# Performance work log

Hardware: AMD Instinct MI355X
Metric: run time of the kernel (lower is better)

## Reference

```python
import jax, jax.numpy as jnp
import numpy as np

NHEAD, DK, DV = 8, 32, 32
GRAPH = [[1,2,3,6,7],[1,2,4],[1,3,5],[2,4],[3,5],[1,6,8,12],[1,7,9,13],[6,8,10],[7,9,13],[8,10],[9,11],[9,12,14],[11,13,15],[12,14,16],[13,15,17],[14,16],[15,17]]
_idx = np.zeros((17,5), np.int32); _val = np.zeros((17,5), bool)
for _i, _nb in enumerate(GRAPH):
    for _j, _n in enumerate(_nb):
        _idx[_i,_j] = _n-1; _val[_i,_j] = True
NBR_IDX = jnp.asarray(_idx)            # (17,5) neighbor table (pad idx 0)
NBR_VALID = jnp.asarray(_val)          # (17,5) valid-neighbor mask
ATT_MASK = jnp.asarray(np.concatenate([_val, np.ones((17,2), bool)], 1))  # (17,7): 5 local + 2 global keys
INV_SQRT_DK = float(1.0/np.sqrt(DK))

def _ln_c(x, g, b, eps=1e-6):
    # LayerNorm over channel axis of (B,C,L)
    m = x.mean(1, keepdims=True)
    v = x.var(1, keepdims=True)
    return (x - m) * jax.lax.rsqrt(v + eps) * g[None,:,None] + b[None,:,None]

def _bn3(x, g, b, eps=1e-5):
    # BatchNorm1d (training batch stats) per channel over (B,L); x:(B,C,L)
    m = x.mean((0,2), keepdims=True)
    v = x.var((0,2), keepdims=True)
    return (x - m) * jax.lax.rsqrt(v + eps) * g[None,:,None] + b[None,:,None]

def _pos_ffn(x, w1, b1, w2, b2, g, b):
    # x:(B,C,L); Linear over C, relu, Linear back, residual, BatchNorm1d
    h = jax.nn.relu(jnp.einsum('bcl,hc->bhl', x, w1) + b1[None,:,None])
    y = jnp.einsum('bhl,ch->bcl', h, w2) + b2[None,:,None] + x
    return _bn3(y, g, b)

def _unfold(t):
    # t:(B,C,17) -> (B,C,5,17): per-node 5-wide neighbor window, zero padded
    g = t[:,:,NBR_IDX]                              # (B,C,17,5)
    g = jnp.where(NBR_VALID[None,None], g, 0.0)
    return jnp.transpose(g, (0,1,3,2))

def _sju(xn, ax, wq,bq,wk,bk,wv,bv, bng,bnb, f1w,f1b,f2w,f2b,fg,fb):
    B, C, L = xn.shape
    q = (jnp.einsum('oc,bcl->bol', wq, xn) + bq[None,:,None]).reshape(B,NHEAD,DK,L)
    kx = jnp.einsum('oc,bcl->bol', wk, xn) + bk[None,:,None]
    vx = jnp.einsum('oc,bcl->bol', wv, xn) + bv[None,:,None]
    k = _unfold(kx).reshape(B,NHEAD,DK,5,L)
    v = _unfold(vx).reshape(B,NHEAD,DV,5,L)
    ak = (jnp.einsum('oc,bcal->boal', wk, ax) + bk[None,:,None,None]).reshape(B,NHEAD,DK,2,L)
    av = (jnp.einsum('oc,bcal->boal', wv, ax) + bv[None,:,None,None]).reshape(B,NHEAD,DV,2,L)
    k = jnp.concatenate([k, ak], 3)                 # (B,H,dk,7,L)
    v = jnp.concatenate([v, av], 3)
    pre = jnp.einsum('bhdl,bhdwl->bhwl', q, k) * INV_SQRT_DK
    pre = jnp.where(ATT_MASK.T[None,None], pre, -jnp.inf)
    a = jax.nn.softmax(pre, axis=2)
    att = jnp.einsum('bhwl,bhdwl->bhdl', a, v).reshape(B,C,L)
    ret = _bn3(xn + att, bng, bnb)
    return _pos_ffn(ret, f1w,f1b,f2w,f2b,fg,fb)

def _sru(x, y, wq,bq,wk,bk,wv,bv, bng,bnb, f1w,f1b,f2w,f2b,fg,fb):
    # x:(B,C) relay, y:(B,C,Ly) keys/values
    B, C = x.shape
    q = (x @ wq.T + bq).reshape(B,NHEAD,DK)
    k = (jnp.einsum('oc,bcl->bol', wk, y) + bk[None,:,None]).reshape(B,NHEAD,DK,-1)
    v = (jnp.einsum('oc,bcl->bol', wv, y) + bv[None,:,None]).reshape(B,NHEAD,DV,-1)
    a = jax.nn.softmax(jnp.einsum('bhd,bhdl->bhl', q, k) * INV_SQRT_DK, axis=2)
    att = jnp.einsum('bhl,bhdl->bhd', a, v).reshape(B,C)
    ret = _bn3((x + att)[:,:,None], bng, bnb)
    return _pos_ffn(ret, f1w,f1b,f2w,f2b,fg,fb)[:,:,0]

def _forward(data, ln_g, ln_b, jq_w, jq_b, jk_w, jk_b, jv_w, jv_b, jbn_g, jbn_b, jf1_w, jf1_b, jf2_w, jf2_b, jfbn_g, jfbn_b, rq_w, rq_b, rk_w, rk_b, rv_w, rv_b, rbn_g, rbn_b, rf1_w, rf1_b, rf2_w, rf2_b, rfbn_g, rfbn_b):
    B, C, V, T = data.shape
    embs = jnp.transpose(data, (0,3,1,2)).reshape(B*T, C, V)   # fold time into batch
    nodes = embs
    relay = embs.mean(2)                                       # (BT,C)
    # ax: per node the 2 extra keys = its own original embedding + relay (fixed across layers)
    ax = jnp.stack([embs, jnp.broadcast_to(relay[:,:,None], embs.shape)], axis=2)  # (BT,C,2,V)
    for i in range(ln_g.shape[0]):
        xn = _ln_c(nodes, ln_g[i], ln_b[i])
        nodes = jax.nn.leaky_relu(_sju(xn, ax, jq_w[i],jq_b[i],jk_w[i],jk_b[i],jv_w[i],jv_b[i],jbn_g[i],jbn_b[i],jf1_w[i],jf1_b[i],jf2_w[i],jf2_b[i],jfbn_g[i],jfbn_b[i]), 0.01)
        y = jnp.concatenate([relay[:,:,None], nodes], axis=2)   # (BT,C,18)
        relay = jax.nn.leaky_relu(_sru(relay, y, rq_w[i],rq_b[i],rk_w[i],rk_b[i],rv_w[i],rv_b[i],rbn_g[i],rbn_b[i],rf1_w[i],rf1_b[i],rf2_w[i],rf2_b[i],rfbn_g[i],rfbn_b[i]), 0.01)
    return jnp.transpose(nodes.reshape(B,T,C,V), (0,2,3,1))

def setup_inputs():
    key = jax.random.key(0)
    Lyr, C, DIN, B, T, V = 2, 256, 1024, 4, 256, 17
    ks = jax.random.split(key, 40)
    ctr = [0]
    def nxt():
        k = ks[ctr[0]]; ctr[0] += 1; return k
    def w(shape, s=0.05):
        return jax.random.normal(nxt(), shape, jnp.float32) * s
    ones = lambda: jnp.ones((Lyr, C), jnp.float32)
    zeros = lambda: jnp.zeros((Lyr, C), jnp.float32)
    inp = {'data': jax.random.normal(nxt(), (B,C,V,T), jnp.float32),
           'ln_g': ones(), 'ln_b': zeros()}
    for p in ('j', 'r'):
        inp[p+'q_w'] = w((Lyr,C,C)); inp[p+'q_b'] = w((Lyr,C))
        inp[p+'k_w'] = w((Lyr,C,C)); inp[p+'k_b'] = w((Lyr,C))
        inp[p+'v_w'] = w((Lyr,C,C)); inp[p+'v_b'] = w((Lyr,C))
        inp[p+'bn_g'] = ones(); inp[p+'bn_b'] = zeros()
        inp[p+'f1_w'] = w((Lyr,DIN,C)); inp[p+'f1_b'] = w((Lyr,DIN))
        inp[p+'f2_w'] = w((Lyr,C,DIN)); inp[p+'f2_b'] = w((Lyr,C))
        inp[p+'fbn_g'] = ones(); inp[p+'fbn_b'] = zeros()
    return inp

def reference(data, ln_g, ln_b, jq_w, jq_b, jk_w, jk_b, jv_w, jv_b, jbn_g, jbn_b, jf1_w, jf1_b, jf2_w, jf2_b, jfbn_g, jfbn_b, rq_w, rq_b, rk_w, rk_b, rv_w, rv_b, rbn_g, rbn_b, rf1_w, rf1_b, rf2_w, rf2_b, rfbn_g, rfbn_b):
    return _forward(data, ln_g, ln_b, jq_w, jq_b, jk_w, jk_b, jv_w, jv_b, jbn_g, jbn_b, jf1_w, jf1_b, jf2_w, jf2_b, jfbn_g, jfbn_b, rq_w, rq_b, rk_w, rk_b, rv_w, rv_b, rbn_g, rbn_b, rf1_w, rf1_b, rf2_w, rf2_b, rfbn_g, rfbn_b)
```

## Files before the change

### kernel.cpp

```cpp
#include <hip/hip_runtime.h>
#include <hip/hip_bf16.h>


using bf16 = __hip_bfloat16;
typedef __attribute__((ext_vector_type(8))) short bf16x8v;
typedef __attribute__((ext_vector_type(4))) float f32x4;

namespace {
constexpr int kBT = 1024;
constexpr int kC = 256;
constexpr int kV = 17;
constexpr int kT = 256;
constexpr int kDIN = 1024;
constexpr int kRows = kBT * kV;
constexpr int kRowsE = kRows + kBT;
constexpr float kInvSqrtDk = 0.17677669529663687f;
constexpr size_t SZ_BIG = (size_t)kRows * kC;
}

__constant__ int c_nbi[17][5] = {
    {0, 1, 2, 5, 6},   {0, 1, 3, 0, 0},   {0, 2, 4, 0, 0},  {1, 3, 0, 0, 0},
    {2, 4, 0, 0, 0},   {0, 5, 7, 11, 0},  {0, 6, 8, 12, 0}, {5, 7, 9, 0, 0},
    {6, 8, 12, 0, 0},  {7, 9, 0, 0, 0},   {8, 10, 0, 0, 0}, {8, 11, 13, 0, 0},
    {10, 12, 14, 0, 0},{11, 13, 15, 0, 0},{12, 14, 16, 0, 0},
    {13, 15, 0, 0, 0}, {14, 16, 0, 0, 0}};
__constant__ int c_ncnt[17] = {5, 3, 3, 2, 2, 4, 4, 3, 3, 2, 2, 3, 3, 3, 3, 2, 2};

__device__ inline float bf2f(unsigned short s) {
  unsigned int u = ((unsigned int)s) << 16;
  float f;
  __builtin_memcpy(&f, &u, 4);
  return f;
}
__device__ inline unsigned short f2bf(float f) {
  unsigned int u;
  __builtin_memcpy(&u, &f, 4);
  unsigned int r = (u + 0x7fffu + ((u >> 16) & 1u)) >> 16;
  return (unsigned short)r;
}
__device__ inline float4 ldbf4(const bf16* p) {
  ushort4 u = *(const ushort4*)p;
  return make_float4(bf2f(u.x), bf2f(u.y), bf2f(u.z), bf2f(u.w));
}
__device__ inline void stbf4(bf16* p, float4 v) {
  ushort4 u = make_ushort4(f2bf(v.x), f2bf(v.y), f2bf(v.z), f2bf(v.w));
  *(ushort4*)p = u;
}
__device__ inline float dot4(float4 a, float4 b) {
  return a.x * b.x + a.y * b.y + a.z * b.z + a.w * b.w;
}

__device__ inline void async16(const bf16* g, bf16* l) {
  __builtin_amdgcn_global_load_lds(
      (const __attribute__((address_space(1))) void*)g,
      (__attribute__((address_space(3))) void*)l, 16, 0, 0);
}

__global__ __launch_bounds__(256) void k_mfma_gemm(
    const bf16* __restrict__ A, const bf16* __restrict__ W,
    const float* __restrict__ bias, const float* __restrict__ res,
    float* __restrict__ outF, bf16* __restrict__ outB,
    int M, int N, int K, int flags) {
  __shared__ bf16 As[128 * 128];
  __shared__ bf16 Bs[128 * 128];
  const int tid = threadIdx.x;
  const int wave = tid >> 6;
  const int lane = tid & 63;
  const int row0 = blockIdx.x * 128;
  const int col0 = blockIdx.y * 128;

  const int sub = lane >> 2;
  const int kq = (lane & 3) * 8;
  const int rg0 = (2 * wave + 0) * 16;
  const int rg1 = (2 * wave + 1) * 16;
  const bf16* ag0 = A + (size_t)(row0 + rg0 + sub) * K + kq;
  const bf16* ag1 = A + (size_t)(row0 + rg1 + sub) * K + kq;
  const bf16* bg0 = W + (size_t)(col0 + rg0 + sub) * K + kq;
  const bf16* bg1 = W + (size_t)(col0 + rg1 + sub) * K + kq;

  const int wm = wave >> 1, wn = wave & 1;
  const int fr = lane & 15;
  const int fk = (lane >> 4) * 8;

  f32x4 acc[4][4];
#pragma unroll
  for (int i = 0; i < 4; ++i)
#pragma unroll
    for (int j = 0; j < 4; ++j) acc[i][j] = (f32x4){0.f, 0.f, 0.f, 0.f};

  for (int k0 = 0; k0 < K; k0 += 128) {
    if (k0) __syncthreads();
#pragma unroll
    for (int kc = 0; kc < 4; ++kc) {
      const int off = k0 + kc * 32;
      async16(ag0 + off, &As[kc * 4096 + rg0 * 32]);
      async16(ag1 + off, &As[kc * 4096 + rg1 * 32]);
      async16(bg0 + off, &Bs[kc * 4096 + rg0 * 32]);
      async16(bg1 + off, &Bs[kc * 4096 + rg1 * 32]);
    }
    __syncthreads();
#pragma unroll
    for (int kc = 0; kc < 4; ++kc) {
      bf16x8v af[4], bfv[4];
#pragma unroll
      for (int i = 0; i < 4; ++i)
        af[i] =
            *(const bf16x8v*)&As[kc * 4096 + (wm * 64 + i * 16 + fr) * 32 + fk];
#pragma unroll
      for (int j = 0; j < 4; ++j)
        bfv[j] =
            *(const bf16x8v*)&Bs[kc * 4096 + (wn * 64 + j * 16 + fr) * 32 + fk];
#pragma unroll
      for (int i = 0; i < 4; ++i)
#pragma unroll
        for (int j = 0; j < 4; ++j)
          acc[i][j] = __builtin_amdgcn_mfma_f32_16x16x32_bf16(af[i], bfv[j],
                                                              acc[i][j], 0, 0,
                                                              0);
    }
  }

  if (flags & 4) {
    unsigned short* cs = (unsigned short*)As;
    __syncthreads();
#pragma unroll
    for (int j = 0; j < 4; ++j) {
      int lc = wn * 64 + j * 16 + fr;
      float bv = bias ? bias[col0 + lc] : 0.f;
#pragma unroll
      for (int i = 0; i < 4; ++i) {
        int lr = wm * 64 + i * 16 + (lane >> 4) * 4;
#pragma unroll
        for (int r = 0; r < 4; ++r) {
          float v = acc[i][j][r] + bv;
          if (flags & 1) v = fmaxf(v, 0.f);
          cs[(lr + r) * 128 + lc] = f2bf(v);
        }
      }
    }
    __syncthreads();
#pragma unroll
    for (int p = 0; p < 8; ++p) {
      int lr = p * 16 + (tid >> 4);
      int lc = (tid & 15) * 8;
      *(bf16x8v*)&outB[(size_t)(row0 + lr) * N + col0 + lc] =
          *(const bf16x8v*)&cs[lr * 128 + lc];
    }
  } else {
    const int crow = row0 + wm * 64;
    const int ccol = col0 + wn * 64;
#pragma unroll
    for (int j = 0; j < 4; ++j) {
      int col = ccol + j * 16 + fr;
      float bv = bias ? bias[col] : 0.f;
#pragma unroll
      for (int i = 0; i < 4; ++i) {
        int rowb = crow + i * 16 + (lane >> 4) * 4;
#pragma unroll
        for (int r = 0; r < 4; ++r) {
          size_t row = (size_t)(rowb + r);
          float v = acc[i][j][r] + bv;
          if (res) v += res[row * N + col];
          if (flags & 1) v = fmaxf(v, 0.f);
          outF[row * N + col] = v;
        }
      }
    }
  }
}

__global__ __launch_bounds__(256) void k_xform_in(const float* __restrict__ data,
                                                  float* __restrict__ nodes,
                                                  bf16* __restrict__ embs_bf) {
  __shared__ float tile[32][33];
  int ct = blockIdx.x * 32, tt = blockIdx.y * 32;
  int bv = blockIdx.z;
  int b = bv / kV, v = bv - b * kV;
  int tx = threadIdx.x & 31, ty = threadIdx.x >> 5;
  for (int i = ty; i < 32; i += 8)
    tile[i][tx] = data[(((size_t)b * kC + ct + i) * kV + v) * kT + tt + tx];
  __syncthreads();
  for (int i = ty; i < 32; i += 8) {
    size_t s = (size_t)b * kT + tt + i;
    size_t idx = (s * kV + v) * kC + ct + tx;
    float val = tile[tx][i];
    nodes[idx] = val;
    embs_bf[idx] = __float2bfloat16(val);
  }
}

__global__ __launch_bounds__(256) void k_xform_out(const float* __restrict__ nodes,
                                                   float* __restrict__ out) {
  __shared__ float tile[32][33];
  int ct = blockIdx.x * 32, tt = blockIdx.y * 32;
  int bv = blockIdx.z;
  int b = bv / kV, v = bv - b * kV;
  int tx = threadIdx.x & 31, ty = threadIdx.x >> 5;
  for (int i = ty; i < 32; i += 8) {
    size_t s = (size_t)b * kT + tt + i;
    tile[i][tx] = nodes[(s * kV + v) * kC + ct + tx];
  }
  __syncthreads();
  for (int i = ty; i < 32; i += 8)
    out[(((size_t)b * kC + ct + i) * kV + v) * kT + tt + tx] = tile[tx][i];
}

__global__ __launch_bounds__(256) void k_relay_init(const float* __restrict__ nodes,
                                                    bf16* __restrict__ relay0_bf) {
  int t = threadIdx.x;
  int s = blockIdx.x * 4 + (t >> 6);
  int c4 = (t & 63) * 4;
  float4 acc = make_float4(0.f, 0.f, 0.f, 0.f);
#pragma unroll
  for (int v = 0; v < kV; ++v) {
    float4 x = *(const float4*)(nodes + ((size_t)s * kV + v) * kC + c4);
    acc.x += x.x; acc.y += x.y; acc.z += x.z; acc.w += x.w;
  }
  float4 r = make_float4(acc.x / 17.f, acc.y / 17.f, acc.z / 17.f, acc.w / 17.f);
  stbf4(relay0_bf + (size_t)s * kC + c4, r);
}

__global__ __launch_bounds__(256) void k_layernorm(const float* __restrict__ X,
                                                   const float* __restrict__ g,
                                                   const float* __restrict__ b,
                                                   float* __restrict__ O,
                                                   bf16* __restrict__ Ob) {
  int t = threadIdx.x;
  int row = blockIdx.x * 4 + (t >> 6);
  int c4 = (t & 63) * 4;
  size_t i = (size_t)row * kC + c4;
  float4 x = *(const float4*)(X + i);
  float s = x.x + x.y + x.z + x.w;
  float q = dot4(x, x);
#pragma unroll
  for (int o = 32; o >= 1; o >>= 1) {
    s += __shfl_xor(s, o);
    q += __shfl_xor(q, o);
  }
  float m = s * (1.f / 256.f);
  float var = q * (1.f / 256.f) - m * m;
  float rs = rsqrtf(var + 1e-6f);
  float4 g4 = *(const float4*)(g + c4);
  float4 b4 = *(const float4*)(b + c4);
  float4 o4 = make_float4((x.x - m) * rs * g4.x + b4.x,
                          (x.y - m) * rs * g4.y + b4.y,
                          (x.z - m) * rs * g4.z + b4.z,
                          (x.w - m) * rs * g4.w + b4.w);
  *(float4*)(O + i) = o4;
  stbf4(Ob + i, o4);
}

__global__ __launch_bounds__(256) void k_attn_sat(const bf16* __restrict__ qkv,
                                                  const bf16* __restrict__ akav,
                                                  float* __restrict__ z) {
  int t = threadIdx.x;
  int rl = blockIdx.x * 4 + (t >> 6);
  int lane = t & 63;
  int s = rl / kV, l = rl - s * kV;
  int c4 = lane * 4;
  float4 q = ldbf4(qkv + (size_t)rl * 768 + c4);
  int cnt = c_ncnt[l];
  float sc[7];
  int nrow[5];
#pragma unroll
  for (int w = 0; w < 5; ++w) {
    nrow[w] = s * kV + c_nbi[l][w];
    float4 k = ldbf4(qkv + (size_t)nrow[w] * 768 + 256 + c4);
    float p = dot4(q, k);
    p += __shfl_xor(p, 1, 8);
    p += __shfl_xor(p, 2, 8);
    p += __shfl_xor(p, 4, 8);
    sc[w] = (w < cnt) ? p * kInvSqrtDk : -1e30f;
  }
  {
    float4 k = ldbf4(akav + (size_t)rl * 1024 + c4);
    float p = dot4(q, k);
    p += __shfl_xor(p, 1, 8);
    p += __shfl_xor(p, 2, 8);
    p += __shfl_xor(p, 4, 8);
    sc[5] = p * kInvSqrtDk;
  }
  {
    float4 k = ldbf4(akav + (size_t)(kRows + s) * 1024 + c4);
    float p = dot4(q, k);
    p += __shfl_xor(p, 1, 8);
    p += __shfl_xor(p, 2, 8);
    p += __shfl_xor(p, 4, 8);
    sc[6] = p * kInvSqrtDk;
  }
  float mx = sc[0];
#pragma unroll
  for (int w = 1; w < 7; ++w) mx = fmaxf(mx, sc[w]);
  float den = 0.f;
#pragma unroll
  for (int w = 0; w < 7; ++w) {
    sc[w] = __expf(sc[w] - mx);
    den += sc[w];
  }
  float inv = 1.f / den;
  float4 acc = make_float4(0.f, 0.f, 0.f, 0.f);
#pragma unroll
  for (int w = 0; w < 5; ++w) {
    float4 v = ldbf4(qkv + (size_t)nrow[w] * 768 + 512 + c4);
    acc.x += sc[w] * v.x; acc.y += sc[w] * v.y;
    acc.z += sc[w] * v.z; acc.w += sc[w] * v.w;
  }
  {
    float4 v = ldbf4(akav + (size_t)rl * 1024 + 256 + c4);
    acc.x += sc[5] * v.x; acc.y += sc[5] * v.y;
    acc.z += sc[5] * v.z; acc.w += sc[5] * v.w;
  }
  {
    float4 v = ldbf4(akav + (size_t)(kRows + s) * 1024 + 256 + c4);
    acc.x += sc[6] * v.x; acc.y += sc[6] * v.y;
    acc.z += sc[6] * v.z; acc.w += sc[6] * v.w;
  }
  size_t zi = (size_t)rl * kC + c4;
  float4 xv = *(const float4*)(z + zi);
  *(float4*)(z + zi) = make_float4(xv.x + acc.x * inv, xv.y + acc.y * inv,
                                   xv.z + acc.z * inv, xv.w + acc.w * inv);
}

__global__ __launch_bounds__(256) void k_bn_partial(const float* __restrict__ A,
                                                    float* __restrict__ part,
                                                    int nb) {
  int c = threadIdx.x, blk = blockIdx.x;
  int lo = blk * 16;
  float s = 0.f, q = 0.f;
#pragma unroll
  for (int r = 0; r < 16; ++r) {
    float v = A[(size_t)(lo + r) * kC + c];
    s += v;
    q += v * v;
  }
  part[(size_t)blk * kC + c] = s;
  part[(size_t)(nb + blk) * kC + c] = q;
}

__global__ __launch_bounds__(256) void k_bn_finalize(const float* __restrict__ part,
                                                     int nb, float inv_n,
                                                     const float* __restrict__ g,
                                                     const float* __restrict__ b,
                                                     float* __restrict__ scale,
                                                     float* __restrict__ shift) {
  int c = blockIdx.x;
  int t = threadIdx.x;
  float s = 0.f, q = 0.f;
  for (int i = t; i < nb; i += 256) {
    s += part[(size_t)i * kC + c];
    q += part[(size_t)(nb + i) * kC + c];
  }
#pragma unroll
  for (int o = 32; o >= 1; o >>= 1) {
    s += __shfl_xor(s, o);
    q += __shfl_xor(q, o);
  }
  __shared__ float ws[4], wq[4];
  int wid = t >> 6;
  if ((t & 63) == 0) { ws[wid] = s; wq[wid] = q; }
  __syncthreads();
  if (t == 0) {
    float S = ws[0] + ws[1] + ws[2] + ws[3];
    float Q = wq[0] + wq[1] + wq[2] + wq[3];
    float m = S * inv_n;
    float var = Q * inv_n - m * m;
    float sc = g[c] * rsqrtf(var + 1e-5f);
    scale[c] = sc;
    shift[c] = b[c] - m * sc;
  }
}

__global__ __launch_bounds__(256) void k_bn_apply(const float* __restrict__ Z,
                                                  const float* __restrict__ scale,
                                                  const float* __restrict__ shift,
                                                  float* __restrict__ outF,
                                                  bf16* __restrict__ outB,
                                                  int leaky) {
  int t = threadIdx.x;
  int row = blockIdx.x * 4 + (t >> 6);
  int c4 = (t & 63) * 4;
  size_t i = (size_t)row * kC + c4;
  float4 z = *(const float4*)(Z + i);
  float4 sc = *(const float4*)(scale + c4);
  float4 sh = *(const float4*)(shift + c4);
  float4 v = make_float4(z.x * sc.x + sh.x, z.y * sc.y + sh.y,
                         z.z * sc.z + sh.z, z.w * sc.w + sh.w);
  if (leaky) {
    v.x = (v.x > 0.f) ? v.x : 0.01f * v.x;
    v.y = (v.y > 0.f) ? v.y : 0.01f * v.y;
    v.z = (v.z > 0.f) ? v.z : 0.01f * v.z;
    v.w = (v.w > 0.f) ? v.w : 0.01f * v.w;
  }
  if (outF) *(float4*)(outF + i) = v;
  if (outB) stbf4(outB + i, v);
}

__global__ __launch_bounds__(256) void k_bn_ln(
    const float* __restrict__ Z, const float* __restrict__ scale,
    const float* __restrict__ shift, const float* __restrict__ g,
    const float* __restrict__ b, float* __restrict__ nodesOut,
    float* __restrict__ xnOut, bf16* __restrict__ actOut) {
  int t = threadIdx.x;
  int row = blockIdx.x * 4 + (t >> 6);
  int c4 = (t & 63) * 4;
  size_t i = (size_t)row * kC + c4;
  float4 z = *(const float4*)(Z + i);
  float4 sc = *(const float4*)(scale + c4);
  float4 sh = *(const float4*)(shift + c4);
  float4 v = make_float4(z.x * sc.x + sh.x, z.y * sc.y + sh.y,
                         z.z * sc.z + sh.z, z.w * sc.w + sh.w);
  v.x = (v.x > 0.f) ? v.x : 0.01f * v.x;
  v.y = (v.y > 0.f) ? v.y : 0.01f * v.y;
  v.z = (v.z > 0.f) ? v.z : 0.01f * v.z;
  v.w = (v.w > 0.f) ? v.w : 0.01f * v.w;
  *(float4*)(nodesOut + i) = v;
  float s = v.x + v.y + v.z + v.w;
  float q = dot4(v, v);
#pragma unroll
  for (int o = 32; o >= 1; o >>= 1) {
    s += __shfl_xor(s, o);
    q += __shfl_xor(q, o);
  }
  float m = s * (1.f / 256.f);
  float var = q * (1.f / 256.f) - m * m;
  float rs = rsqrtf(var + 1e-6f);
  float4 g4 = *(const float4*)(g + c4);
  float4 b4 = *(const float4*)(b + c4);
  float4 o4 = make_float4((v.x - m) * rs * g4.x + b4.x,
                          (v.y - m) * rs * g4.y + b4.y,
                          (v.z - m) * rs * g4.z + b4.z,
                          (v.w - m) * rs * g4.w + b4.w);
  *(float4*)(xnOut + i) = o4;
  stbf4(actOut + i, o4);
}

struct CvtTab {
  const float* src[12];
  bf16* dst[12];
  int n[12];
};
__global__ __launch_bounds__(256) void k_cvt_multi(CvtTab t) {
  int c = blockIdx.y;
  int i = (blockIdx.x * 256 + threadIdx.x) * 4;
  if (i >= t.n[c]) return;
  float4 v = *(const float4*)(t.src[c] + i);
  stbf4(t.dst[c] + i, v);
}

struct BiasTab {
  const float* src[10];
  float* dst[10];
};
__global__ __launch_bounds__(256) void k_bias_cat(BiasTab t) {
  t.dst[blockIdx.x][threadIdx.x] = t.src[blockIdx.x][threadIdx.x];
}

extern "C" void kernel_launch(void* const* d_in, const int* in_sizes, int n_in,
                              void* d_out, int out_size, void* d_ws, size_t ws_size,
                              hipStream_t stream) {
  const float* data = (const float*)d_in[0];
  const float* ln_g = (const float*)d_in[1];
  const float* ln_b = (const float*)d_in[2];
  const float* jq_w = (const float*)d_in[3];
  const float* jq_b = (const float*)d_in[4];
  const float* jk_w = (const float*)d_in[5];
  const float* jk_b = (const float*)d_in[6];
  const float* jv_w = (const float*)d_in[7];
  const float* jv_b = (const float*)d_in[8];
  const float* jbn_g = (const float*)d_in[9];
  const float* jbn_b = (const float*)d_in[10];
  const float* jf1_w = (const float*)d_in[11];
  const float* jf1_b = (const float*)d_in[12];
  const float* jf2_w = (const float*)d_in[13];
  const float* jf2_b = (const float*)d_in[14];
  const float* jfbn_g = (const float*)d_in[15];
  const float* jfbn_b = (const float*)d_in[16];
  float* out = (float*)d_out;

  float* f = (float*)d_ws;
  float* nodes = f;    f += SZ_BIG;
  float* xn = f;       f += SZ_BIG;
  float* part = f;     f += 2 * 1088 * kC;
  float* scale = f;    f += kC;
  float* shift = f;    f += kC;
  float* cb_jqkv = f;  f += 2 * 768;
  float* cb_kv4 = f;   f += 1024;

  bf16* bfa = (bf16*)f;
  bf16* act_bf = bfa;   bfa += SZ_BIG;
  bf16* embsX_bf = bfa; bfa += (size_t)kRowsE * kC;
  bf16* P = bfa;        bfa += (size_t)kRows * kDIN;
  bf16* akavBuf = bfa;  bfa += (size_t)kRowsE * 1024;
  bf16* Wjqkv = bfa;    bfa += 2 * 768 * 256;
  bf16* Wkv4 = bfa;     bfa += 1024 * 256;
  bf16* Wjf1 = bfa;     bfa += 2 * 1024 * 256;
  bf16* Wjf2 = bfa;     bfa += 2 * 256 * 1024;

  bf16* relay0_bf = embsX_bf + SZ_BIG;
  bf16* qkv_bf = P;
  bf16* h_bf = P;
  float* y2 = xn;

  auto gemm = [&](const bf16* A, const bf16* W, const float* bias,
                  const float* res, float* oF, bf16* oB, int M, int N, int K,
                  int flags) {
    dim3 g(M / 128, N / 128);
    k_mfma_gemm<<<g, 256, 0, stream>>>(A, W, bias, res, oF, oB, M, N, K, flags);
  };

  {
    CvtTab t;
    for (int i = 0; i < 2; ++i) {
      const size_t om = (size_t)i * kC * kC;
      const float* s3[3] = {jq_w + om, jk_w + om, jv_w + om};
      bf16* d3[3] = {Wjqkv + (size_t)i * 768 * 256,
                     Wjqkv + (size_t)i * 768 * 256 + 65536,
                     Wjqkv + (size_t)i * 768 * 256 + 131072};
      for (int j = 0; j < 3; ++j) {
        t.src[i * 3 + j] = s3[j];
        t.dst[i * 3 + j] = d3[j];
        t.n[i * 3 + j] = 65536;
      }
    }
    t.src[6] = jk_w;                 t.dst[6] = Wkv4;               t.n[6] = 65536;
    t.src[7] = jv_w;                 t.dst[7] = Wkv4 + 65536;       t.n[7] = 65536;
    t.src[8] = jk_w + (size_t)65536; t.dst[8] = Wkv4 + 131072;      t.n[8] = 65536;
    t.src[9] = jv_w + (size_t)65536; t.dst[9] = Wkv4 + 196608;      t.n[9] = 65536;
    t.src[10] = jf1_w; t.dst[10] = Wjf1; t.n[10] = 2 * 1024 * 256;
    t.src[11] = jf2_w; t.dst[11] = Wjf2; t.n[11] = 2 * 256 * 1024;
    k_cvt_multi<<<dim3(512, 12), 256, 0, stream>>>(t);
  }
  {
    BiasTab t;
    for (int i = 0; i < 2; ++i) {
      t.src[i * 3 + 0] = jq_b + (size_t)i * kC;
      t.src[i * 3 + 1] = jk_b + (size_t)i * kC;
      t.src[i * 3 + 2] = jv_b + (size_t)i * kC;
      t.dst[i * 3 + 0] = cb_jqkv + i * 768;
      t.dst[i * 3 + 1] = cb_jqkv + i * 768 + 256;
      t.dst[i * 3 + 2] = cb_jqkv + i * 768 + 512;
    }
    t.src[6] = jk_b;       t.dst[6] = cb_kv4;
    t.src[7] = jv_b;       t.dst[7] = cb_kv4 + 256;
    t.src[8] = jk_b + kC;  t.dst[8] = cb_kv4 + 512;
    t.src[9] = jv_b + kC;  t.dst[9] = cb_kv4 + 768;
    k_bias_cat<<<10, 256, 0, stream>>>(t);
  }

  k_xform_in<<<dim3(8, 8, 4 * kV), 256, 0, stream>>>(data, nodes, embsX_bf);
  k_relay_init<<<kBT / 4, 256, 0, stream>>>(nodes, relay0_bf);

  gemm(embsX_bf, Wkv4, cb_kv4, nullptr, nullptr, akavBuf, kRowsE, 1024, 256, 4);

  k_layernorm<<<kRows / 4, 256, 0, stream>>>(nodes, ln_g, ln_b, xn, act_bf);

  for (int i = 0; i < 2; ++i) {
    const size_t ob = (size_t)i * kC, ofb1 = (size_t)i * kDIN;
    const bf16* Wj = Wjqkv + (size_t)i * 768 * 256;
    const bf16* Wf1 = Wjf1 + (size_t)i * 1024 * 256;
    const bf16* Wf2 = Wjf2 + (size_t)i * 256 * 1024;
    const float* cbj = cb_jqkv + i * 768;
    const int nb = kRows / 16;

    gemm(act_bf, Wj, cbj, nullptr, nullptr, qkv_bf, kRows, 768, 256, 4);
    k_attn_sat<<<kRows / 4, 256, 0, stream>>>(qkv_bf, akavBuf + (size_t)i * 512,
                                              xn);
    k_bn_partial<<<nb, 256, 0, stream>>>(xn, part, nb);
    k_bn_finalize<<<kC, 256, 0, stream>>>(part, nb, 1.f / kRows, jbn_g + ob,
                                          jbn_b + ob, scale, shift);
    k_bn_apply<<<kRows / 4, 256, 0, stream>>>(xn, scale, shift, nodes, act_bf,
                                              0);
    gemm(act_bf, Wf1, jf1_b + ofb1, nullptr, nullptr, h_bf, kRows, 1024, 256,
         4 | 1);
    gemm(h_bf, Wf2, jf2_b + ob, nodes, y2, nullptr, kRows, 256, 1024, 2);
    k_bn_partial<<<nb, 256, 0, stream>>>(y2, part, nb);
    k_bn_finalize<<<kC, 256, 0, stream>>>(part, nb, 1.f / kRows, jfbn_g + ob,
                                          jfbn_b + ob, scale, shift);
    if (i == 0) {
      k_bn_ln<<<kRows / 4, 256, 0, stream>>>(y2, scale, shift, ln_g + kC,
                                             ln_b + kC, nodes, xn, act_bf);
    } else {
      k_bn_apply<<<kRows / 4, 256, 0, stream>>>(y2, scale, shift, nodes,
                                                nullptr, 1);
    }
  }

  k_xform_out<<<dim3(8, 8, 4 * kV), 256, 0, stream>>>(nodes, out);
  (void)in_sizes; (void)n_in; (void)out_size; (void)ws_size;
}
```

Baseline: 438.2 us.

## Double-buffer GEMM LDS tiles with 64-wide K steps and template K

Rewrites the MFMA GEMM main loop to use two 64-wide K LDS buffers. The load of the next tile is issued asynchronously while the current tile is computed, which is meant to hide global-to-LDS latency. K becomes a template parameter (256 or 1024) so the loop bounds and strides are compile-time constants. The total LDS footprint stays the same, but there is one barrier per 64-wide K step instead of two per 128, so synchronisation is more frequent, and the correctness of the async-load overlap relies on the barrier placement.

```diff
diff --git a/kernel.cpp b/kernel.cpp
--- a/kernel.cpp
+++ b/kernel.cpp
@@ -56,13 +56,13 @@
       (__attribute__((address_space(3))) void*)l, 16, 0, 0);
 }
 
+template <int KT>
 __global__ __launch_bounds__(256) void k_mfma_gemm(
     const bf16* __restrict__ A, const bf16* __restrict__ W,
     const float* __restrict__ bias, const float* __restrict__ res,
-    float* __restrict__ outF, bf16* __restrict__ outB,
-    int M, int N, int K, int flags) {
-  __shared__ bf16 As[128 * 128];
-  __shared__ bf16 Bs[128 * 128];
+    float* __restrict__ outF, bf16* __restrict__ outB, int N, int flags) {
+  __shared__ bf16 As[2][128 * 64];
+  __shared__ bf16 Bs[2][128 * 64];
   const int tid = threadIdx.x;
   const int wave = tid >> 6;
   const int lane = tid & 63;
@@ -73,10 +73,10 @@
   const int kq = (lane & 3) * 8;
   const int rg0 = (2 * wave + 0) * 16;
   const int rg1 = (2 * wave + 1) * 16;
-  const bf16* ag0 = A + (size_t)(row0 + rg0 + sub) * K + kq;
-  const bf16* ag1 = A + (size_t)(row0 + rg1 + sub) * K + kq;
-  const bf16* bg0 = W + (size_t)(col0 + rg0 + sub) * K + kq;
-  const bf16* bg1 = W + (size_t)(col0 + rg1 + sub) * K + kq;
+  const bf16* ag0 = A + (size_t)(row0 + rg0 + sub) * KT + kq;
+  const bf16* ag1 = A + (size_t)(row0 + rg1 + sub) * KT + kq;
+  const bf16* bg0 = W + (size_t)(col0 + rg0 + sub) * KT + kq;
+  const bf16* bg1 = W + (size_t)(col0 + rg1 + sub) * KT + kq;
 
   const int wm = wave >> 1, wn = wave & 1;
   const int fr = lane & 15;
@@ -88,28 +88,34 @@
 #pragma unroll
     for (int j = 0; j < 4; ++j) acc[i][j] = (f32x4){0.f, 0.f, 0.f, 0.f};
 
-  for (int k0 = 0; k0 < K; k0 += 128) {
-    if (k0) __syncthreads();
-#pragma unroll
-    for (int kc = 0; kc < 4; ++kc) {
-      const int off = k0 + kc * 32;
-      async16(ag0 + off, &As[kc * 4096 + rg0 * 32]);
-      async16(ag1 + off, &As[kc * 4096 + rg1 * 32]);
-      async16(bg0 + off, &Bs[kc * 4096 + rg0 * 32]);
-      async16(bg1 + off, &Bs[kc * 4096 + rg1 * 32]);
-    }
-    __syncthreads();
-#pragma unroll
-    for (int kc = 0; kc < 4; ++kc) {
+#define STAGE64(buf, koff)                                   \
+  do {                                                       \
+    _Pragma("unroll") for (int kc = 0; kc < 2; ++kc) {       \
+      const int off = (koff) + kc * 32;                      \
+      async16(ag0 + off, &As[(buf)][kc * 4096 + rg0 * 32]);  \
+      async16(ag1 + off, &As[(buf)][kc * 4096 + rg1 * 32]);  \
+      async16(bg0 + off, &Bs[(buf)][kc * 4096 + rg0 * 32]);  \
+      async16(bg1 + off, &Bs[(buf)][kc * 4096 + rg1 * 32]);  \
+    }                                                        \
+  } while (0)
+
+  STAGE64(0, 0);
+  __syncthreads();
+
+  for (int k0 = 0; k0 < KT; k0 += 64) {
+    const int cur = (k0 >> 6) & 1;
+    if (k0 + 64 < KT) STAGE64(cur ^ 1, k0 + 64);
+#pragma unroll
+    for (int kc = 0; kc < 2; ++kc) {
       bf16x8v af[4], bfv[4];
 #pragma unroll
       for (int i = 0; i < 4; ++i)
-        af[i] =
-            *(const bf16x8v*)&As[kc * 4096 + (wm * 64 + i * 16 + fr) * 32 + fk];
+        af[i] = *(const bf16x8v*)&As[cur][kc * 4096 +
+                                          (wm * 64 + i * 16 + fr) * 32 + fk];
 #pragma unroll
       for (int j = 0; j < 4; ++j)
-        bfv[j] =
-            *(const bf16x8v*)&Bs[kc * 4096 + (wn * 64 + j * 16 + fr) * 32 + fk];
+        bfv[j] = *(const bf16x8v*)&Bs[cur][kc * 4096 +
+                                           (wn * 64 + j * 16 + fr) * 32 + fk];
 #pragma unroll
       for (int i = 0; i < 4; ++i)
 #pragma unroll
@@ -118,11 +124,12 @@
                                                               acc[i][j], 0, 0,
                                                               0);
     }
-  }
+    __syncthreads();
+  }
+#undef STAGE64
 
   if (flags & 4) {
     unsigned short* cs = (unsigned short*)As;
-    __syncthreads();
 #pragma unroll
     for (int j = 0; j < 4; ++j) {
       int lc = wn * 64 + j * 16 + fr;
@@ -505,7 +512,12 @@
                   const float* res, float* oF, bf16* oB, int M, int N, int K,
                   int flags) {
     dim3 g(M / 128, N / 128);
-    k_mfma_gemm<<<g, 256, 0, stream>>>(A, W, bias, res, oF, oB, M, N, K, flags);
+    if (K == 256)
+      k_mfma_gemm<256><<<g, 256, 0, stream>>>(A, W, bias, res, oF, oB, N,
+                                              flags);
+    else
+      k_mfma_gemm<1024><<<g, 256, 0, stream>>>(A, W, bias, res, oF, oB, N,
+                                               flags);
   };
 
   {
```

New measurement: 441.8 us. About the same (+0.8%).
